# Kernel tuning notes

Measured on AMD Instinct MI355X. Metric: run time of the kernel, lower is better.

## Reference

```python
import jax, jax.numpy as jnp
import numpy as np

B, LQ, LK = 16, 256, 256
DQ = DK = DV = H = 256


def setup_inputs() -> dict:
    key = jax.random.key(0)
    ks = jax.random.split(key, 7)
    queries = jax.random.normal(ks[0], (B, LQ, DQ), dtype=jnp.float32)
    keys = jax.random.normal(ks[1], (B, LK, DK), dtype=jnp.float32)
    values = jax.random.normal(ks[2], (B, LK, DV), dtype=jnp.float32)
    valid_lens = jax.random.randint(ks[3], (B,), 1, LK + 1).astype(jnp.int32)
    W_q = jax.random.normal(ks[4], (DQ, H), dtype=jnp.float32) / np.sqrt(DQ)
    W_k = jax.random.normal(ks[5], (DK, H), dtype=jnp.float32) / np.sqrt(DK)
    w_v = jax.random.normal(ks[6], (H,), dtype=jnp.float32) / np.sqrt(H)
    return {"queries": queries, "keys": keys, "values": values,
            "valid_lens": valid_lens, "W_q": W_q, "W_k": W_k, "w_v": w_v}


def reference(queries, keys, values, valid_lens, W_q, W_k, w_v):
    # Project queries and keys to the hidden size (no bias)
    q = jnp.einsum('bqd,dh->bqh', queries, W_q)          # (B, Lq, H)
    k = jnp.einsum('bkd,dh->bkh', keys, W_k)             # (B, Lk, H)
    # Broadcast-add, tanh, then contract with w_v -> scores (B, Lq, Lk)
    features = jnp.tanh(q[:, :, None, :] + k[:, None, :, :])  # (B, Lq, Lk, H)
    scores = jnp.einsum('bqkh,h->bqk', features, w_v)
    # Masked softmax over last axis: positions >= valid_len get -1e6
    mask = jnp.arange(scores.shape[-1]) < valid_lens[:, None, None]  # (B,1,Lk) bcast
    scores = jnp.where(mask, scores, jnp.float32(-1e6))
    attn = jax.nn.softmax(scores, axis=-1)
    # Dropout is identity at inference (training=False)
    return jnp.einsum('bqk,bkv->bqv', attn, values)      # (B, Lq, Dv)
```

## Files before the change

kernel.cpp:

```cpp
#include <hip/hip_runtime.h>

using bf16x8 = __attribute__((ext_vector_type(8))) __bf16;
using f32x4  = __attribute__((ext_vector_type(4))) float;
using f32x2  = __attribute__((ext_vector_type(2))) float;
using us8    = __attribute__((ext_vector_type(8))) unsigned short;

#define TWO_LOG2E 2.8853900817779268f
#define LOG2E 1.4426950408889634f

__device__ __forceinline__ unsigned short f2bf(float x) {
  unsigned int u = __float_as_uint(x);
  u = (u + 0x7fffu + ((u >> 16) & 1u)) >> 16;
  return (unsigned short)u;
}
__device__ __forceinline__ float bf2f(unsigned short h) {
  return __uint_as_float(((unsigned int)h) << 16);
}
__device__ __forceinline__ f32x2 pk_fma(f32x2 a, f32x2 b, f32x2 c) {
  return __builtin_elementwise_fma(a, b, c);
}

__global__ __launch_bounds__(256) void tcast_kernel(
    const float* __restrict__ Wq, const float* __restrict__ Wk,
    const float* __restrict__ vals, const float* __restrict__ wv,
    const int* __restrict__ vlens,
    unsigned short* __restrict__ wt_hi, unsigned short* __restrict__ wt_lo,
    unsigned short* __restrict__ vt_hi, unsigned short* __restrict__ vt_lo,
    float* __restrict__ wv2, float* __restrict__ Wsum,
    int* __restrict__ ctr, int* __restrict__ cum) {
  if (blockIdx.x == 0) {
    int t = threadIdx.x;
    wv2[t] = -2.0f * wv[t];
    if (t < 64) {
      float s = wv[t] + wv[t + 64] + wv[t + 128] + wv[t + 192];
#pragma unroll
      for (int off = 1; off < 64; off <<= 1) s += __shfl_xor(s, off, 64);
      if (t == 0) Wsum[0] = s;
    }
    if (t == 0) {
      ctr[0] = 0;
      int c = 0;
      for (int b = 0; b < 16; ++b) {
        cum[b] = c;
        c += ((vlens[b] + 31) >> 5) << 3;
      }
      cum[16] = c;
    }
  }
  __shared__ float tile[32][33];
  int m = blockIdx.x >> 6;
  int ts = blockIdx.x & 63;
  int R0 = (ts >> 3) << 5, C0 = (ts & 7) << 5;
  const float* src = (m == 0) ? Wq : (m == 1) ? Wk : (vals + ((m - 2) << 16));
  int r = threadIdx.x >> 3, c4 = (threadIdx.x & 7) << 2;
  float4 v = *(const float4*)(src + (R0 + r) * 256 + C0 + c4);
  tile[r][c4] = v.x; tile[r][c4 + 1] = v.y; tile[r][c4 + 2] = v.z; tile[r][c4 + 3] = v.w;
  __syncthreads();
  float o0 = tile[c4 + 0][r], o1 = tile[c4 + 1][r];
  float o2 = tile[c4 + 2][r], o3 = tile[c4 + 3][r];
  unsigned short h0 = f2bf(o0), h1 = f2bf(o1), h2 = f2bf(o2), h3 = f2bf(o3);
  int base = ((m < 2) ? (m << 16) : ((m - 2) << 16)) + (C0 + r) * 256 + R0 + c4;
  unsigned short* dh = (m < 2) ? wt_hi : vt_hi;
  unsigned short* dl = (m < 2) ? wt_lo : vt_lo;
  *(ushort4*)(dh + base) = make_ushort4(h0, h1, h2, h3);
  *(ushort4*)(dl + base) = make_ushort4(f2bf(o0 - bf2f(h0)), f2bf(o1 - bf2f(h1)),
                                        f2bf(o2 - bf2f(h2)), f2bf(o3 - bf2f(h3)));
}

__global__ __launch_bounds__(256, 4) void proj_kernel(
    const float* __restrict__ q, const float* __restrict__ kk,
    const unsigned short* __restrict__ w_hi, const unsigned short* __restrict__ w_lo,
    const int* __restrict__ vlens, float* __restrict__ Rq, float* __restrict__ RkT) {
  int wave = threadIdx.x >> 6, lane = threadIdx.x & 63;
  int mt = (blockIdx.x << 1) + (wave & 1);
  int m0 = mt << 4;
  int g = mt >> 8;
  if (g) {
    int bb = (m0 >> 8) & 15;
    if ((m0 & 255) >= vlens[bb]) return;
  }
  int r = lane & 15, qd = lane >> 4;
  int row = m0 + r;
  const float* A = (g == 0) ? (q + row * 256) : (kk + (row - 4096) * 256);
  int nbase = (blockIdx.y << 6) + ((wave >> 1) << 5);
  int boff0 = (g << 16) + (nbase + r) * 256 + qd * 8;
  int boff1 = boff0 + (16 << 8);
  f32x4 acc0 = {0.f, 0.f, 0.f, 0.f}, acc1 = {0.f, 0.f, 0.f, 0.f};
#pragma unroll
  for (int kh = 0; kh < 2; ++kh) {
    bf16x8 ah[4], al[4];
#pragma unroll
    for (int s = 0; s < 4; ++s) {
      const float* p = A + qd * 8 + (kh * 4 + s) * 32;
      float4 f0 = *(const float4*)p;
      float4 f1 = *(const float4*)(p + 4);
      float fv[8] = {f0.x, f0.y, f0.z, f0.w, f1.x, f1.y, f1.z, f1.w};
#pragma unroll
      for (int j = 0; j < 8; ++j) {
        __bf16 h = (__bf16)fv[j];
        ah[s][j] = h;
        al[s][j] = (__bf16)(fv[j] - (float)h);
      }
    }
#pragma unroll
    for (int s = 0; s < 4; ++s) {
      int off = (kh * 4 + s) * 32;
      bf16x8 bh0 = *(const bf16x8*)(w_hi + boff0 + off);
      bf16x8 bl0 = *(const bf16x8*)(w_lo + boff0 + off);
      acc0 = __builtin_amdgcn_mfma_f32_16x16x32_bf16(ah[s], bh0, acc0, 0, 0, 0);
      acc0 = __builtin_amdgcn_mfma_f32_16x16x32_bf16(ah[s], bl0, acc0, 0, 0, 0);
      acc0 = __builtin_amdgcn_mfma_f32_16x16x32_bf16(al[s], bh0, acc0, 0, 0, 0);
      bf16x8 bh1 = *(const bf16x8*)(w_hi + boff1 + off);
      bf16x8 bl1 = *(const bf16x8*)(w_lo + boff1 + off);
      acc1 = __builtin_amdgcn_mfma_f32_16x16x32_bf16(ah[s], bh1, acc1, 0, 0, 0);
      acc1 = __builtin_amdgcn_mfma_f32_16x16x32_bf16(ah[s], bl1, acc1, 0, 0, 0);
      acc1 = __builtin_amdgcn_mfma_f32_16x16x32_bf16(al[s], bh1, acc1, 0, 0, 0);
    }
  }
#pragma unroll
  for (int tI = 0; tI < 2; ++tI) {
    f32x4 acc = tI ? acc1 : acc0;
    int n0 = nbase + (tI << 4);
    f32x4 ex;
#pragma unroll
    for (int i = 0; i < 4; ++i) {
      float l = acc[i] * TWO_LOG2E;
      l = fminf(fmaxf(l, -27.f), 27.f);
      ex[i] = __builtin_amdgcn_exp2f(l);
    }
    if (g == 0) {
#pragma unroll
      for (int i = 0; i < 4; ++i)
        Rq[(m0 + qd * 4 + i) * 256 + n0 + r] = ex[i];
    } else {
      int b = (m0 >> 8) & 15;
      int kloc = (m0 & 255) + qd * 4;
      *(f32x4*)(RkT + (b << 16) + (n0 + r) * 256 + kloc) = ex;
    }
  }
}

__global__ __launch_bounds__(256, 2) void scores_kernel(
    const float* __restrict__ Rq, const float* __restrict__ RkT,
    const float* __restrict__ wv2, const float* __restrict__ Wsum,
    const int* __restrict__ cum, int* __restrict__ ctr,
    float* __restrict__ sc) {
  __shared__ __align__(16) float rqs[32 * 76];
  __shared__ __align__(16) float kT[64 * 34];
  __shared__ int s_item;
  const int t = threadIdx.x;
  const int tq = t >> 4, tk = t & 15;
  const int sr = t >> 3, shb = (t & 7) << 3;
  const int hrow = t >> 2, kq = (t & 3) << 3;
  const int total = cum[16];
  const float ws = Wsum[0];

  for (;;) {
    __syncthreads();
    if (t == 0) s_item = atomicAdd(ctr, 1);
    __syncthreads();
    const int w = s_item;
    if (w >= total) return;
    int b = 0;
    while (cum[b + 1] <= w) ++b;
    const int local = w - cum[b];
    const int k0 = (local >> 3) << 5;
    const int q0 = (local & 7) << 5;
    const int qrow = (b << 8) + q0;
    f32x2 a0 = {0.f, 0.f}, a1 = {0.f, 0.f};

    for (int hc = 0; hc < 4; ++hc) {
      if (hc) __syncthreads();
      const float* gq = Rq + (qrow + sr) * 256 + (hc << 6) + shb;
      *(float4*)(rqs + sr * 76 + shb)     = *(const float4*)gq;
      *(float4*)(rqs + sr * 76 + shb + 4) = *(const float4*)(gq + 4);
      const float* gk = RkT + (b << 16) + ((hc << 6) + hrow) * 256 + k0 + kq;
      *(float4*)(kT + hrow * 34 + kq)     = *(const float4*)gk;
      *(float4*)(kT + hrow * 34 + kq + 4) = *(const float4*)(gk + 4);
      __syncthreads();
#pragma unroll 2
      for (int h = 0; h < 64; h += 4) {
        f32x4 qa = *(const f32x4*)(rqs + tq * 76 + h);
        f32x4 qb = *(const f32x4*)(rqs + (tq + 16) * 76 + h);
        f32x4 wm = *(const f32x4*)(wv2 + (hc << 6) + h);
#pragma unroll
        for (int j = 0; j < 4; ++j) {
          f32x2 rk = *(const f32x2*)(kT + (h + j) * 34 + (tk << 1));
          f32x2 wj = (f32x2)(wm[j]);
          f32x2 d0 = pk_fma(rk, (f32x2)(qa[j]), (f32x2)(1.0f));
          f32x2 d1 = pk_fma(rk, (f32x2)(qb[j]), (f32x2)(1.0f));
          f32x2 r0, r1;
          r0.x = __uint_as_float(0x7EF311C3u - __float_as_uint(d0.x));
          r0.y = __uint_as_float(0x7EF311C3u - __float_as_uint(d0.y));
          r1.x = __uint_as_float(0x7EF311C3u - __float_as_uint(d1.x));
          r1.y = __uint_as_float(0x7EF311C3u - __float_as_uint(d1.y));
          r0 = r0 * pk_fma(-d0, r0, (f32x2)(2.0f));
          r1 = r1 * pk_fma(-d1, r1, (f32x2)(2.0f));
          a0 = pk_fma(r0, wj, a0);
          a1 = pk_fma(r1, wj, a1);
        }
      }
    }
    a0 += (f32x2)(ws);
    a1 += (f32x2)(ws);
    *(f32x2*)(sc + ((qrow + tq) << 8) + k0 + (tk << 1)) = a0;
    *(f32x2*)(sc + ((qrow + tq + 16) << 8) + k0 + (tk << 1)) = a1;
  }
}

__global__ __launch_bounds__(256) void av_fused_kernel(
    const float* __restrict__ sc, const int* __restrict__ vlens,
    const unsigned short* __restrict__ vhi, const unsigned short* __restrict__ vlo,
    float* __restrict__ out) {
  __shared__ __align__(16) unsigned short athi[16 * 264];
  const int wave = threadIdx.x >> 6, lane = threadIdx.x & 63;
  const int b = blockIdx.x;
  const int m0 = blockIdx.y << 4;
  const int vl = vlens[b];

  {
    int row = (wave << 2) + (lane & 3);
    int c0 = (lane >> 2) << 4;
    const float* srow = sc + ((b << 8) + m0 + row) * 256 + c0;
    float4 x0 = *(const float4*)(srow);
    float4 x1 = *(const float4*)(srow + 4);
    float4 x2 = *(const float4*)(srow + 8);
    float4 x3 = *(const float4*)(srow + 12);
    float p[16] = {x0.x, x0.y, x0.z, x0.w, x1.x, x1.y, x1.z, x1.w,
                   x2.x, x2.y, x2.z, x2.w, x3.x, x3.y, x3.z, x3.w};
#pragma unroll
    for (int i = 0; i < 16; ++i)
      if (c0 + i >= vl) p[i] = -1e6f;
    float mx = p[0];
#pragma unroll
    for (int i = 1; i < 16; ++i) mx = fmaxf(mx, p[i]);
#pragma unroll
    for (int off = 4; off <= 32; off <<= 1) mx = fmaxf(mx, __shfl_xor(mx, off, 64));
    float sm = 0.f;
#pragma unroll
    for (int i = 0; i < 16; ++i) {
      p[i] = __builtin_amdgcn_exp2f((p[i] - mx) * LOG2E);
      sm += p[i];
    }
#pragma unroll
    for (int off = 4; off <= 32; off <<= 1) sm += __shfl_xor(sm, off, 64);
    float rs = __builtin_amdgcn_rcpf(sm);
    us8 vh[2];
#pragma unroll
    for (int i = 0; i < 16; ++i) vh[i >> 3][i & 7] = f2bf(p[i] * rs);
    *(us8*)(athi + row * 264 + c0)     = vh[0];
    *(us8*)(athi + row * 264 + c0 + 8) = vh[1];
  }
  __syncthreads();

  const int r = lane & 15, qd = lane >> 4;
  const int smax = (vl + 31) >> 5;
  const int nb = wave << 6;
  const int boff = (b << 16) + (nb + r) * 256 + qd * 8;
  f32x4 acc[4] = {{0.f,0.f,0.f,0.f},{0.f,0.f,0.f,0.f},
                  {0.f,0.f,0.f,0.f},{0.f,0.f,0.f,0.f}};
  for (int s = 0; s < smax; ++s) {
    bf16x8 pa = *(const bf16x8*)(athi + r * 264 + qd * 8 + s * 32);
#pragma unroll
    for (int tI = 0; tI < 4; ++tI) {
      bf16x8 bh = *(const bf16x8*)(vhi + boff + (tI << 12) + s * 32);
      bf16x8 bl = *(const bf16x8*)(vlo + boff + (tI << 12) + s * 32);
      acc[tI] = __builtin_amdgcn_mfma_f32_16x16x32_bf16(pa, bh, acc[tI], 0, 0, 0);
      acc[tI] = __builtin_amdgcn_mfma_f32_16x16x32_bf16(pa, bl, acc[tI], 0, 0, 0);
    }
  }
#pragma unroll
  for (int tI = 0; tI < 4; ++tI)
#pragma unroll
    for (int i = 0; i < 4; ++i)
      out[(b << 16) + (m0 + qd * 4 + i) * 256 + nb + (tI << 4) + r] = acc[tI][i];
}

extern "C" void kernel_launch(void* const* d_in, const int* in_sizes, int n_in,
                              void* d_out, int out_size, void* d_ws, size_t ws_size,
                              hipStream_t stream) {
  const float* queries = (const float*)d_in[0];
  const float* keys    = (const float*)d_in[1];
  const float* values  = (const float*)d_in[2];
  const int*   vlens   = (const int*)d_in[3];
  const float* Wq      = (const float*)d_in[4];
  const float* Wk      = (const float*)d_in[5];
  const float* wv      = (const float*)d_in[6];
  float* out = (float*)d_out;
  char* ws = (char*)d_ws;

  unsigned short* wt_hi = (unsigned short*)(ws + 0);
  unsigned short* wt_lo = (unsigned short*)(ws + 262144);
  unsigned short* vt_hi = (unsigned short*)(ws + 524288);
  unsigned short* vt_lo = (unsigned short*)(ws + 2621440);
  float*          Rq    = (float*)(ws + 4718592);
  float*          RkT   = (float*)(ws + 8912896);
  float*          sc    = (float*)(ws + 13107200);
  float*          wv2   = (float*)(ws + 17301504);
  float*          Wsum  = (float*)(ws + 17302528);
  int*            ctr   = (int*)(ws + 17302532);
  int*            cum   = (int*)(ws + 17302536);

  tcast_kernel<<<1152, 256, 0, stream>>>(Wq, Wk, values, wv, vlens,
                                         wt_hi, wt_lo, vt_hi, vt_lo, wv2, Wsum,
                                         ctr, cum);
  proj_kernel<<<dim3(256, 4), 256, 0, stream>>>(queries, keys, wt_hi, wt_lo,
                                                vlens, Rq, RkT);
  scores_kernel<<<512, 256, 0, stream>>>(Rq, RkT, wv2, Wsum, cum, ctr, sc);
  av_fused_kernel<<<dim3(16, 16), 256, 0, stream>>>(sc, vlens, vt_hi, vt_lo, out);
}
```

Baseline: 134.3 us.

## Fuse all stages into persistent megakernel with grid-wide barriers

Replaces four kernel launches with one persistent kernel sized to occupancy, separating stages with atomic grid barriers. The values transpose/cast is moved into the dynamic work queue of the scores stage so it overlaps score computation, and the AV stage is split into quarter-width column tiles to raise parallelism. This removes launch gaps and idle tails between kernels, at the cost of spin barriers, a memset launch, and reliance on all blocks being co-resident.

```diff
diff --git a/kernel.cpp b/kernel.cpp
--- a/kernel.cpp
+++ b/kernel.cpp
@@ -20,16 +20,35 @@
   return __builtin_elementwise_fma(a, b, c);
 }
 
-__global__ __launch_bounds__(256) void tcast_kernel(
-    const float* __restrict__ Wq, const float* __restrict__ Wk,
+__device__ __forceinline__ void gsync(int* bar, int idx, int nblk) {
+  __syncthreads();
+  if (threadIdx.x == 0) {
+    __threadfence();
+    __hip_atomic_fetch_add(bar + idx, 1, __ATOMIC_ACQ_REL, __HIP_MEMORY_SCOPE_AGENT);
+    while (__hip_atomic_load(bar + idx, __ATOMIC_ACQUIRE, __HIP_MEMORY_SCOPE_AGENT) < nblk)
+      __builtin_amdgcn_s_sleep(2);
+  }
+  __syncthreads();
+}
+
+__global__ __launch_bounds__(256, 4) void mega_kernel(
+    const float* __restrict__ q, const float* __restrict__ kk,
     const float* __restrict__ vals, const float* __restrict__ wv,
     const int* __restrict__ vlens,
+    const float* __restrict__ Wq, const float* __restrict__ Wk,
     unsigned short* __restrict__ wt_hi, unsigned short* __restrict__ wt_lo,
     unsigned short* __restrict__ vt_hi, unsigned short* __restrict__ vt_lo,
-    float* __restrict__ wv2, float* __restrict__ Wsum,
-    int* __restrict__ ctr, int* __restrict__ cum) {
+    float* __restrict__ wv2, float* __restrict__ Wsum, int* __restrict__ cum,
+    float* __restrict__ Rq, float* __restrict__ RkT, float* __restrict__ sc,
+    float* __restrict__ out, int* __restrict__ bar) {
+  __shared__ __align__(16) char smem[18448];
+  float* rqs   = (float*)smem;
+  float* kT    = (float*)(smem + 9728);
+  int*   s_item = (int*)(smem + 18432);
+  const int nblk = gridDim.x;
+  const int t = threadIdx.x;
+
   if (blockIdx.x == 0) {
-    int t = threadIdx.x;
     wv2[t] = -2.0f * wv[t];
     if (t < 64) {
       float s = wv[t] + wv[t + 64] + wv[t + 128] + wv[t + 192];
@@ -38,7 +57,6 @@
       if (t == 0) Wsum[0] = s;
     }
     if (t == 0) {
-      ctr[0] = 0;
       int c = 0;
       for (int b = 0; b < 16; ++b) {
         cum[b] = c;
@@ -47,233 +65,238 @@
       cum[16] = c;
     }
   }
-  __shared__ float tile[32][33];
-  int m = blockIdx.x >> 6;
-  int ts = blockIdx.x & 63;
-  int R0 = (ts >> 3) << 5, C0 = (ts & 7) << 5;
-  const float* src = (m == 0) ? Wq : (m == 1) ? Wk : (vals + ((m - 2) << 16));
-  int r = threadIdx.x >> 3, c4 = (threadIdx.x & 7) << 2;
-  float4 v = *(const float4*)(src + (R0 + r) * 256 + C0 + c4);
-  tile[r][c4] = v.x; tile[r][c4 + 1] = v.y; tile[r][c4 + 2] = v.z; tile[r][c4 + 3] = v.w;
-  __syncthreads();
-  float o0 = tile[c4 + 0][r], o1 = tile[c4 + 1][r];
-  float o2 = tile[c4 + 2][r], o3 = tile[c4 + 3][r];
-  unsigned short h0 = f2bf(o0), h1 = f2bf(o1), h2 = f2bf(o2), h3 = f2bf(o3);
-  int base = ((m < 2) ? (m << 16) : ((m - 2) << 16)) + (C0 + r) * 256 + R0 + c4;
-  unsigned short* dh = (m < 2) ? wt_hi : vt_hi;
-  unsigned short* dl = (m < 2) ? wt_lo : vt_lo;
-  *(ushort4*)(dh + base) = make_ushort4(h0, h1, h2, h3);
-  *(ushort4*)(dl + base) = make_ushort4(f2bf(o0 - bf2f(h0)), f2bf(o1 - bf2f(h1)),
-                                        f2bf(o2 - bf2f(h2)), f2bf(o3 - bf2f(h3)));
-}
-
-__global__ __launch_bounds__(256, 4) void proj_kernel(
-    const float* __restrict__ q, const float* __restrict__ kk,
-    const unsigned short* __restrict__ w_hi, const unsigned short* __restrict__ w_lo,
-    const int* __restrict__ vlens, float* __restrict__ Rq, float* __restrict__ RkT) {
-  int wave = threadIdx.x >> 6, lane = threadIdx.x & 63;
-  int mt = (blockIdx.x << 1) + (wave & 1);
-  int m0 = mt << 4;
-  int g = mt >> 8;
-  if (g) {
-    int bb = (m0 >> 8) & 15;
-    if ((m0 & 255) >= vlens[bb]) return;
-  }
-  int r = lane & 15, qd = lane >> 4;
-  int row = m0 + r;
-  const float* A = (g == 0) ? (q + row * 256) : (kk + (row - 4096) * 256);
-  int nbase = (blockIdx.y << 6) + ((wave >> 1) << 5);
-  int boff0 = (g << 16) + (nbase + r) * 256 + qd * 8;
-  int boff1 = boff0 + (16 << 8);
-  f32x4 acc0 = {0.f, 0.f, 0.f, 0.f}, acc1 = {0.f, 0.f, 0.f, 0.f};
-#pragma unroll
-  for (int kh = 0; kh < 2; ++kh) {
-    bf16x8 ah[4], al[4];
-#pragma unroll
-    for (int s = 0; s < 4; ++s) {
-      const float* p = A + qd * 8 + (kh * 4 + s) * 32;
-      float4 f0 = *(const float4*)p;
-      float4 f1 = *(const float4*)(p + 4);
-      float fv[8] = {f0.x, f0.y, f0.z, f0.w, f1.x, f1.y, f1.z, f1.w};
-#pragma unroll
-      for (int j = 0; j < 8; ++j) {
-        __bf16 h = (__bf16)fv[j];
-        ah[s][j] = h;
-        al[s][j] = (__bf16)(fv[j] - (float)h);
-      }
-    }
-#pragma unroll
-    for (int s = 0; s < 4; ++s) {
-      int off = (kh * 4 + s) * 32;
-      bf16x8 bh0 = *(const bf16x8*)(w_hi + boff0 + off);
-      bf16x8 bl0 = *(const bf16x8*)(w_lo + boff0 + off);
-      acc0 = __builtin_amdgcn_mfma_f32_16x16x32_bf16(ah[s], bh0, acc0, 0, 0, 0);
-      acc0 = __builtin_amdgcn_mfma_f32_16x16x32_bf16(ah[s], bl0, acc0, 0, 0, 0);
-      acc0 = __builtin_amdgcn_mfma_f32_16x16x32_bf16(al[s], bh0, acc0, 0, 0, 0);
-      bf16x8 bh1 = *(const bf16x8*)(w_hi + boff1 + off);
-      bf16x8 bl1 = *(const bf16x8*)(w_lo + boff1 + off);
-      acc1 = __builtin_amdgcn_mfma_f32_16x16x32_bf16(ah[s], bh1, acc1, 0, 0, 0);
-      acc1 = __builtin_amdgcn_mfma_f32_16x16x32_bf16(ah[s], bl1, acc1, 0, 0, 0);
-      acc1 = __builtin_amdgcn_mfma_f32_16x16x32_bf16(al[s], bh1, acc1, 0, 0, 0);
-    }
-  }
-#pragma unroll
-  for (int tI = 0; tI < 2; ++tI) {
-    f32x4 acc = tI ? acc1 : acc0;
-    int n0 = nbase + (tI << 4);
-    f32x4 ex;
-#pragma unroll
-    for (int i = 0; i < 4; ++i) {
-      float l = acc[i] * TWO_LOG2E;
-      l = fminf(fmaxf(l, -27.f), 27.f);
-      ex[i] = __builtin_amdgcn_exp2f(l);
-    }
-    if (g == 0) {
-#pragma unroll
-      for (int i = 0; i < 4; ++i)
-        Rq[(m0 + qd * 4 + i) * 256 + n0 + r] = ex[i];
-    } else {
-      int b = (m0 >> 8) & 15;
-      int kloc = (m0 & 255) + qd * 4;
-      *(f32x4*)(RkT + (b << 16) + (n0 + r) * 256 + kloc) = ex;
-    }
-  }
-}
-
-__global__ __launch_bounds__(256, 2) void scores_kernel(
-    const float* __restrict__ Rq, const float* __restrict__ RkT,
-    const float* __restrict__ wv2, const float* __restrict__ Wsum,
-    const int* __restrict__ cum, int* __restrict__ ctr,
-    float* __restrict__ sc) {
-  __shared__ __align__(16) float rqs[32 * 76];
-  __shared__ __align__(16) float kT[64 * 34];
-  __shared__ int s_item;
-  const int t = threadIdx.x;
-  const int tq = t >> 4, tk = t & 15;
-  const int sr = t >> 3, shb = (t & 7) << 3;
-  const int hrow = t >> 2, kq = (t & 3) << 3;
-  const int total = cum[16];
-  const float ws = Wsum[0];
-
-  for (;;) {
+  if (blockIdx.x < 128) {
+    float (*tile)[33] = (float(*)[33])smem;
+    int m = blockIdx.x >> 6, ts = blockIdx.x & 63;
+    int R0 = (ts >> 3) << 5, C0 = (ts & 7) << 5;
+    const float* src = m ? Wk : Wq;
+    int r = t >> 3, c4 = (t & 7) << 2;
+    float4 v = *(const float4*)(src + (R0 + r) * 256 + C0 + c4);
+    tile[r][c4] = v.x; tile[r][c4 + 1] = v.y; tile[r][c4 + 2] = v.z; tile[r][c4 + 3] = v.w;
     __syncthreads();
-    if (t == 0) s_item = atomicAdd(ctr, 1);
+    float o0 = tile[c4 + 0][r], o1 = tile[c4 + 1][r];
+    float o2 = tile[c4 + 2][r], o3 = tile[c4 + 3][r];
+    unsigned short h0 = f2bf(o0), h1 = f2bf(o1), h2 = f2bf(o2), h3 = f2bf(o3);
+    int base = (m << 16) + (C0 + r) * 256 + R0 + c4;
+    *(ushort4*)(wt_hi + base) = make_ushort4(h0, h1, h2, h3);
+    *(ushort4*)(wt_lo + base) = make_ushort4(f2bf(o0 - bf2f(h0)), f2bf(o1 - bf2f(h1)),
+                                             f2bf(o2 - bf2f(h2)), f2bf(o3 - bf2f(h3)));
+  }
+  gsync(bar, 0, nblk);
+
+  for (int j = blockIdx.x; j < 1024; j += nblk) {
+    int wave = t >> 6, lane = t & 63;
+    int mt = ((j & 255) << 1) + (wave & 1);
+    int m0 = mt << 4;
+    int g = mt >> 8;
+    if (g) {
+      int bb = (m0 >> 8) & 15;
+      if ((m0 & 255) >= vlens[bb]) continue;
+    }
+    int r = lane & 15, qd = lane >> 4;
+    int row = m0 + r;
+    const float* A = (g == 0) ? (q + row * 256) : (kk + (row - 4096) * 256);
+    int nbase = ((j >> 8) << 6) + ((wave >> 1) << 5);
+    int boff0 = (g << 16) + (nbase + r) * 256 + qd * 8;
+    int boff1 = boff0 + (16 << 8);
+    f32x4 acc0 = {0.f, 0.f, 0.f, 0.f}, acc1 = {0.f, 0.f, 0.f, 0.f};
+#pragma unroll
+    for (int kh = 0; kh < 2; ++kh) {
+      bf16x8 ah[4], al[4];
+#pragma unroll
+      for (int s = 0; s < 4; ++s) {
+        const float* p = A + qd * 8 + (kh * 4 + s) * 32;
+        float4 f0 = *(const float4*)p;
+        float4 f1 = *(const float4*)(p + 4);
+        float fv[8] = {f0.x, f0.y, f0.z, f0.w, f1.x, f1.y, f1.z, f1.w};
+#pragma unroll
+        for (int jj = 0; jj < 8; ++jj) {
+          __bf16 h = (__bf16)fv[jj];
+          ah[s][jj] = h;
+          al[s][jj] = (__bf16)(fv[jj] - (float)h);
+        }
+      }
+#pragma unroll
+      for (int s = 0; s < 4; ++s) {
+        int off = (kh * 4 + s) * 32;
+        bf16x8 bh0 = *(const bf16x8*)(wt_hi + boff0 + off);
+        bf16x8 bl0 = *(const bf16x8*)(wt_lo + boff0 + off);
+        acc0 = __builtin_amdgcn_mfma_f32_16x16x32_bf16(ah[s], bh0, acc0, 0, 0, 0);
+        acc0 = __builtin_amdgcn_mfma_f32_16x16x32_bf16(ah[s], bl0, acc0, 0, 0, 0);
+        acc0 = __builtin_amdgcn_mfma_f32_16x16x32_bf16(al[s], bh0, acc0, 0, 0, 0);
+        bf16x8 bh1 = *(const bf16x8*)(wt_hi + boff1 + off);
+        bf16x8 bl1 = *(const bf16x8*)(wt_lo + boff1 + off);
+        acc1 = __builtin_amdgcn_mfma_f32_16x16x32_bf16(ah[s], bh1, acc1, 0, 0, 0);
+        acc1 = __builtin_amdgcn_mfma_f32_16x16x32_bf16(ah[s], bl1, acc1, 0, 0, 0);
+        acc1 = __builtin_amdgcn_mfma_f32_16x16x32_bf16(al[s], bh1, acc1, 0, 0, 0);
+      }
+    }
+#pragma unroll
+    for (int tI = 0; tI < 2; ++tI) {
+      f32x4 acc = tI ? acc1 : acc0;
+      int n0 = nbase + (tI << 4);
+      f32x4 ex;
+#pragma unroll
+      for (int i = 0; i < 4; ++i) {
+        float l = acc[i] * TWO_LOG2E;
+        l = fminf(fmaxf(l, -27.f), 27.f);
+        ex[i] = __builtin_amdgcn_exp2f(l);
+      }
+      if (g == 0) {
+#pragma unroll
+        for (int i = 0; i < 4; ++i)
+          Rq[(m0 + qd * 4 + i) * 256 + n0 + r] = ex[i];
+      } else {
+        int b = (m0 >> 8) & 15;
+        int kloc = (m0 & 255) + qd * 4;
+        *(f32x4*)(RkT + (b << 16) + (n0 + r) * 256 + kloc) = ex;
+      }
+    }
+  }
+  gsync(bar, 1, nblk);
+
+  {
+    const int tq = t >> 4, tk = t & 15;
+    const int sr = t >> 3, shb = (t & 7) << 3;
+    const int hrow = t >> 2, kq = (t & 3) << 3;
+    int* ctr = bar + 3;
+    const int S = cum[16];
+    const int total = S + 1024;
+    const float wsum = Wsum[0];
+
+    for (;;) {
+      __syncthreads();
+      if (t == 0) s_item[0] = atomicAdd(ctr, 1);
+      __syncthreads();
+      const int w = s_item[0];
+      if (w >= total) break;
+      if (w < S) {
+        int b = 0;
+        while (cum[b + 1] <= w) ++b;
+        const int local = w - cum[b];
+        const int k0 = (local >> 3) << 5;
+        const int q0 = (local & 7) << 5;
+        const int qrow = (b << 8) + q0;
+        f32x2 a0 = {0.f, 0.f}, a1 = {0.f, 0.f};
+
+        for (int hc = 0; hc < 4; ++hc) {
+          if (hc) __syncthreads();
+          const float* gq = Rq + (qrow + sr) * 256 + (hc << 6) + shb;
+          *(float4*)(rqs + sr * 76 + shb)     = *(const float4*)gq;
+          *(float4*)(rqs + sr * 76 + shb + 4) = *(const float4*)(gq + 4);
+          const float* gk = RkT + (b << 16) + ((hc << 6) + hrow) * 256 + k0 + kq;
+          *(float4*)(kT + hrow * 34 + kq)     = *(const float4*)gk;
+          *(float4*)(kT + hrow * 34 + kq + 4) = *(const float4*)(gk + 4);
+          __syncthreads();
+#pragma unroll 2
+          for (int h = 0; h < 64; h += 4) {
+            f32x4 qa = *(const f32x4*)(rqs + tq * 76 + h);
+            f32x4 qb = *(const f32x4*)(rqs + (tq + 16) * 76 + h);
+            f32x4 wm = *(const f32x4*)(wv2 + (hc << 6) + h);
+#pragma unroll
+            for (int jj = 0; jj < 4; ++jj) {
+              f32x2 rk = *(const f32x2*)(kT + (h + jj) * 34 + (tk << 1));
+              f32x2 wj = (f32x2)(wm[jj]);
+              f32x2 d0 = pk_fma(rk, (f32x2)(qa[jj]), (f32x2)(1.0f));
+              f32x2 d1 = pk_fma(rk, (f32x2)(qb[jj]), (f32x2)(1.0f));
+              f32x2 r0, r1;
+              r0.x = __uint_as_float(0x7EF311C3u - __float_as_uint(d0.x));
+              r0.y = __uint_as_float(0x7EF311C3u - __float_as_uint(d0.y));
+              r1.x = __uint_as_float(0x7EF311C3u - __float_as_uint(d1.x));
+              r1.y = __uint_as_float(0x7EF311C3u - __float_as_uint(d1.y));
+              r0 = r0 * pk_fma(-d0, r0, (f32x2)(2.0f));
+              r1 = r1 * pk_fma(-d1, r1, (f32x2)(2.0f));
+              a0 = pk_fma(r0, wj, a0);
+              a1 = pk_fma(r1, wj, a1);
+            }
+          }
+        }
+        a0 += (f32x2)(wsum);
+        a1 += (f32x2)(wsum);
+        *(f32x2*)(sc + ((qrow + tq) << 8) + k0 + (tk << 1)) = a0;
+        *(f32x2*)(sc + ((qrow + tq + 16) << 8) + k0 + (tk << 1)) = a1;
+      } else {
+        float (*tile)[33] = (float(*)[33])smem;
+        int jv = w - S;
+        int m = jv >> 6, ts = jv & 63;
+        int R0 = (ts >> 3) << 5, C0 = (ts & 7) << 5;
+        const float* src = vals + (m << 16);
+        int r = t >> 3, c4 = (t & 7) << 2;
+        float4 v = *(const float4*)(src + (R0 + r) * 256 + C0 + c4);
+        tile[r][c4] = v.x; tile[r][c4 + 1] = v.y; tile[r][c4 + 2] = v.z; tile[r][c4 + 3] = v.w;
+        __syncthreads();
+        float o0 = tile[c4 + 0][r], o1 = tile[c4 + 1][r];
+        float o2 = tile[c4 + 2][r], o3 = tile[c4 + 3][r];
+        unsigned short h0 = f2bf(o0), h1 = f2bf(o1), h2 = f2bf(o2), h3 = f2bf(o3);
+        int base = (m << 16) + (C0 + r) * 256 + R0 + c4;
+        *(ushort4*)(vt_hi + base) = make_ushort4(h0, h1, h2, h3);
+        *(ushort4*)(vt_lo + base) = make_ushort4(f2bf(o0 - bf2f(h0)), f2bf(o1 - bf2f(h1)),
+                                                 f2bf(o2 - bf2f(h2)), f2bf(o3 - bf2f(h3)));
+      }
+    }
+  }
+  gsync(bar, 2, nblk);
+
+  for (int j = blockIdx.x; j < 1024; j += nblk) {
     __syncthreads();
-    const int w = s_item;
-    if (w >= total) return;
-    int b = 0;
-    while (cum[b + 1] <= w) ++b;
-    const int local = w - cum[b];
-    const int k0 = (local >> 3) << 5;
-    const int q0 = (local & 7) << 5;
-    const int qrow = (b << 8) + q0;
-    f32x2 a0 = {0.f, 0.f}, a1 = {0.f, 0.f};
-
-    for (int hc = 0; hc < 4; ++hc) {
-      if (hc) __syncthreads();
-      const float* gq = Rq + (qrow + sr) * 256 + (hc << 6) + shb;
-      *(float4*)(rqs + sr * 76 + shb)     = *(const float4*)gq;
-      *(float4*)(rqs + sr * 76 + shb + 4) = *(const float4*)(gq + 4);
-      const float* gk = RkT + (b << 16) + ((hc << 6) + hrow) * 256 + k0 + kq;
-      *(float4*)(kT + hrow * 34 + kq)     = *(const float4*)gk;
-      *(float4*)(kT + hrow * 34 + kq + 4) = *(const float4*)(gk + 4);
-      __syncthreads();
-#pragma unroll 2
-      for (int h = 0; h < 64; h += 4) {
-        f32x4 qa = *(const f32x4*)(rqs + tq * 76 + h);
-        f32x4 qb = *(const f32x4*)(rqs + (tq + 16) * 76 + h);
-        f32x4 wm = *(const f32x4*)(wv2 + (hc << 6) + h);
-#pragma unroll
-        for (int j = 0; j < 4; ++j) {
-          f32x2 rk = *(const f32x2*)(kT + (h + j) * 34 + (tk << 1));
-          f32x2 wj = (f32x2)(wm[j]);
-          f32x2 d0 = pk_fma(rk, (f32x2)(qa[j]), (f32x2)(1.0f));
-          f32x2 d1 = pk_fma(rk, (f32x2)(qb[j]), (f32x2)(1.0f));
-          f32x2 r0, r1;
-          r0.x = __uint_as_float(0x7EF311C3u - __float_as_uint(d0.x));
-          r0.y = __uint_as_float(0x7EF311C3u - __float_as_uint(d0.y));
-          r1.x = __uint_as_float(0x7EF311C3u - __float_as_uint(d1.x));
-          r1.y = __uint_as_float(0x7EF311C3u - __float_as_uint(d1.y));
-          r0 = r0 * pk_fma(-d0, r0, (f32x2)(2.0f));
-          r1 = r1 * pk_fma(-d1, r1, (f32x2)(2.0f));
-          a0 = pk_fma(r0, wj, a0);
-          a1 = pk_fma(r1, wj, a1);
-        }
-      }
-    }
-    a0 += (f32x2)(ws);
-    a1 += (f32x2)(ws);
-    *(f32x2*)(sc + ((qrow + tq) << 8) + k0 + (tk << 1)) = a0;
-    *(f32x2*)(sc + ((qrow + tq + 16) << 8) + k0 + (tk << 1)) = a1;
-  }
-}
-
-__global__ __launch_bounds__(256) void av_fused_kernel(
-    const float* __restrict__ sc, const int* __restrict__ vlens,
-    const unsigned short* __restrict__ vhi, const unsigned short* __restrict__ vlo,
-    float* __restrict__ out) {
-  __shared__ __align__(16) unsigned short athi[16 * 264];
-  const int wave = threadIdx.x >> 6, lane = threadIdx.x & 63;
-  const int b = blockIdx.x;
-  const int m0 = blockIdx.y << 4;
-  const int vl = vlens[b];
-
-  {
-    int row = (wave << 2) + (lane & 3);
-    int c0 = (lane >> 2) << 4;
-    const float* srow = sc + ((b << 8) + m0 + row) * 256 + c0;
-    float4 x0 = *(const float4*)(srow);
-    float4 x1 = *(const float4*)(srow + 4);
-    float4 x2 = *(const float4*)(srow + 8);
-    float4 x3 = *(const float4*)(srow + 12);
-    float p[16] = {x0.x, x0.y, x0.z, x0.w, x1.x, x1.y, x1.z, x1.w,
-                   x2.x, x2.y, x2.z, x2.w, x3.x, x3.y, x3.z, x3.w};
-#pragma unroll
-    for (int i = 0; i < 16; ++i)
-      if (c0 + i >= vl) p[i] = -1e6f;
-    float mx = p[0];
-#pragma unroll
-    for (int i = 1; i < 16; ++i) mx = fmaxf(mx, p[i]);
-#pragma unroll
-    for (int off = 4; off <= 32; off <<= 1) mx = fmaxf(mx, __shfl_xor(mx, off, 64));
-    float sm = 0.f;
-#pragma unroll
-    for (int i = 0; i < 16; ++i) {
-      p[i] = __builtin_amdgcn_exp2f((p[i] - mx) * LOG2E);
-      sm += p[i];
-    }
-#pragma unroll
-    for (int off = 4; off <= 32; off <<= 1) sm += __shfl_xor(sm, off, 64);
-    float rs = __builtin_amdgcn_rcpf(sm);
-    us8 vh[2];
-#pragma unroll
-    for (int i = 0; i < 16; ++i) vh[i >> 3][i & 7] = f2bf(p[i] * rs);
-    *(us8*)(athi + row * 264 + c0)     = vh[0];
-    *(us8*)(athi + row * 264 + c0 + 8) = vh[1];
-  }
-  __syncthreads();
-
-  const int r = lane & 15, qd = lane >> 4;
-  const int smax = (vl + 31) >> 5;
-  const int nb = wave << 6;
-  const int boff = (b << 16) + (nb + r) * 256 + qd * 8;
-  f32x4 acc[4] = {{0.f,0.f,0.f,0.f},{0.f,0.f,0.f,0.f},
-                  {0.f,0.f,0.f,0.f},{0.f,0.f,0.f,0.f}};
-  for (int s = 0; s < smax; ++s) {
-    bf16x8 pa = *(const bf16x8*)(athi + r * 264 + qd * 8 + s * 32);
-#pragma unroll
-    for (int tI = 0; tI < 4; ++tI) {
-      bf16x8 bh = *(const bf16x8*)(vhi + boff + (tI << 12) + s * 32);
-      bf16x8 bl = *(const bf16x8*)(vlo + boff + (tI << 12) + s * 32);
-      acc[tI] = __builtin_amdgcn_mfma_f32_16x16x32_bf16(pa, bh, acc[tI], 0, 0, 0);
-      acc[tI] = __builtin_amdgcn_mfma_f32_16x16x32_bf16(pa, bl, acc[tI], 0, 0, 0);
-    }
-  }
-#pragma unroll
-  for (int tI = 0; tI < 4; ++tI)
+    unsigned short* athi = (unsigned short*)smem;
+    const int wave = t >> 6, lane = t & 63;
+    const int b = j & 15;
+    const int m0 = ((j >> 4) & 15) << 4;
+    const int quad = j >> 8;
+    const int vl = vlens[b];
+
+    {
+      int row = (wave << 2) + (lane & 3);
+      int c0 = (lane >> 2) << 4;
+      const float* srow = sc + ((b << 8) + m0 + row) * 256 + c0;
+      float4 x0 = *(const float4*)(srow);
+      float4 x1 = *(const float4*)(srow + 4);
+      float4 x2 = *(const float4*)(srow + 8);
+      float4 x3 = *(const float4*)(srow + 12);
+      float p[16] = {x0.x, x0.y, x0.z, x0.w, x1.x, x1.y, x1.z, x1.w,
+                     x2.x, x2.y, x2.z, x2.w, x3.x, x3.y, x3.z, x3.w};
+#pragma unroll
+      for (int i = 0; i < 16; ++i)
+        if (c0 + i >= vl) p[i] = -1e6f;
+      float mx = p[0];
+#pragma unroll
+      for (int i = 1; i < 16; ++i) mx = fmaxf(mx, p[i]);
+#pragma unroll
+      for (int off = 4; off <= 32; off <<= 1) mx = fmaxf(mx, __shfl_xor(mx, off, 64));
+      float sm = 0.f;
+#pragma unroll
+      for (int i = 0; i < 16; ++i) {
+        p[i] = __builtin_amdgcn_exp2f((p[i] - mx) * LOG2E);
+        sm += p[i];
+      }
+#pragma unroll
+      for (int off = 4; off <= 32; off <<= 1) sm += __shfl_xor(sm, off, 64);
+      float rs = __builtin_amdgcn_rcpf(sm);
+      us8 vh[2];
+#pragma unroll
+      for (int i = 0; i < 16; ++i) vh[i >> 3][i & 7] = f2bf(p[i] * rs);
+      *(us8*)(athi + row * 264 + c0)     = vh[0];
+      *(us8*)(athi + row * 264 + c0 + 8) = vh[1];
+    }
+    __syncthreads();
+
+    const int r = lane & 15, qd = lane >> 4;
+    const int smax = (vl + 31) >> 5;
+    const int n0 = (quad << 6) + (wave << 4);
+    const int boff = (b << 16) + (n0 + r) * 256 + qd * 8;
+    f32x4 acc = {0.f, 0.f, 0.f, 0.f};
+    for (int s = 0; s < smax; ++s) {
+      bf16x8 pa = *(const bf16x8*)(athi + r * 264 + qd * 8 + s * 32);
+      bf16x8 bh = *(const bf16x8*)(vt_hi + boff + s * 32);
+      bf16x8 bl = *(const bf16x8*)(vt_lo + boff + s * 32);
+      acc = __builtin_amdgcn_mfma_f32_16x16x32_bf16(pa, bh, acc, 0, 0, 0);
+      acc = __builtin_amdgcn_mfma_f32_16x16x32_bf16(pa, bl, acc, 0, 0, 0);
+    }
 #pragma unroll
     for (int i = 0; i < 4; ++i)
-      out[(b << 16) + (m0 + qd * 4 + i) * 256 + nb + (tI << 4) + r] = acc[tI][i];
+      out[(b << 16) + (m0 + qd * 4 + i) * 256 + n0 + r] = acc[i];
+  }
 }
 
 extern "C" void kernel_launch(void* const* d_in, const int* in_sizes, int n_in,
@@ -298,14 +321,29 @@
   float*          sc    = (float*)(ws + 13107200);
   float*          wv2   = (float*)(ws + 17301504);
   float*          Wsum  = (float*)(ws + 17302528);
-  int*            ctr   = (int*)(ws + 17302532);
   int*            cum   = (int*)(ws + 17302536);
-
-  tcast_kernel<<<1152, 256, 0, stream>>>(Wq, Wk, values, wv, vlens,
-                                         wt_hi, wt_lo, vt_hi, vt_lo, wv2, Wsum,
-                                         ctr, cum);
-  proj_kernel<<<dim3(256, 4), 256, 0, stream>>>(queries, keys, wt_hi, wt_lo,
-                                                vlens, Rq, RkT);
-  scores_kernel<<<512, 256, 0, stream>>>(Rq, RkT, wv2, Wsum, cum, ctr, sc);
-  av_fused_kernel<<<dim3(16, 16), 256, 0, stream>>>(sc, vlens, vt_hi, vt_lo, out);
-}
+  int*            bar   = (int*)(ws + 17302604);
+
+  static int nblk = 0;
+  if (nblk == 0) {
+    int per = 0;
+    if (hipOccupancyMaxActiveBlocksPerMultiprocessor(&per, mega_kernel, 256, 0) != hipSuccess
+        || per < 1) per = 1;
+    if (per > 4) per = 4;
+    int cus = 256;
+    hipDeviceProp_t prop;
+    int dev = 0;
+    if (hipGetDevice(&dev) == hipSuccess &&
+        hipGetDeviceProperties(&prop, dev) == hipSuccess &&
+        prop.multiProcessorCount > 0)
+      cus = prop.multiProcessorCount;
+    long g = (long)per * cus;
+    nblk = (int)(g > 1024 ? 1024 : g);
+    if (nblk < 1) nblk = 1;
+  }
+
+  hipMemsetAsync(ws + 17302604, 0, 16, stream);
+  mega_kernel<<<nblk, 256, 0, stream>>>(queries, keys, values, wv, vlens, Wq, Wk,
+                                        wt_hi, wt_lo, vt_hi, vt_lo, wv2, Wsum, cum,
+                                        Rq, RkT, sc, out, bar);
+}
```

Result: slower. 425.6 us (+216.9%).

## Fuse scores, masked softmax and AV into one per-query-tile kernel

Applied to the files above, without the earlier changes.

Merges the scores kernel and the softmax/AV kernel into one kernel with one block per (batch, 16-query tile). Each block loops over only the valid key tiles, keeps scores in shared memory, then runs softmax and the bf16 MFMA AV product. This removes the global score buffer round trip, one launch, and the atomic work-queue setup. In exchange, each thread now computes one query row instead of two, so there is less instruction-level parallelism. The grid is fixed at 256 blocks with no dynamic balancing, so batches with long valid lengths become the critical path.

```diff
diff --git a/kernel.cpp b/kernel.cpp
--- a/kernel.cpp
+++ b/kernel.cpp
@@ -23,11 +23,9 @@
 __global__ __launch_bounds__(256) void tcast_kernel(
     const float* __restrict__ Wq, const float* __restrict__ Wk,
     const float* __restrict__ vals, const float* __restrict__ wv,
-    const int* __restrict__ vlens,
     unsigned short* __restrict__ wt_hi, unsigned short* __restrict__ wt_lo,
     unsigned short* __restrict__ vt_hi, unsigned short* __restrict__ vt_lo,
-    float* __restrict__ wv2, float* __restrict__ Wsum,
-    int* __restrict__ ctr, int* __restrict__ cum) {
+    float* __restrict__ wv2, float* __restrict__ Wsum) {
   if (blockIdx.x == 0) {
     int t = threadIdx.x;
     wv2[t] = -2.0f * wv[t];
@@ -36,15 +34,6 @@
 #pragma unroll
       for (int off = 1; off < 64; off <<= 1) s += __shfl_xor(s, off, 64);
       if (t == 0) Wsum[0] = s;
-    }
-    if (t == 0) {
-      ctr[0] = 0;
-      int c = 0;
-      for (int b = 0; b < 16; ++b) {
-        cum[b] = c;
-        c += ((vlens[b] + 31) >> 5) << 3;
-      }
-      cum[16] = c;
     }
   }
   __shared__ float tile[32][33];
@@ -140,88 +129,69 @@
   }
 }
 
-__global__ __launch_bounds__(256, 2) void scores_kernel(
+__global__ __launch_bounds__(256) void sav_kernel(
     const float* __restrict__ Rq, const float* __restrict__ RkT,
     const float* __restrict__ wv2, const float* __restrict__ Wsum,
-    const int* __restrict__ cum, int* __restrict__ ctr,
-    float* __restrict__ sc) {
-  __shared__ __align__(16) float rqs[32 * 76];
+    const int* __restrict__ vlens,
+    const unsigned short* __restrict__ vhi, const unsigned short* __restrict__ vlo,
+    float* __restrict__ out) {
+  __shared__ __align__(16) float rqs[16 * 260];
   __shared__ __align__(16) float kT[64 * 34];
-  __shared__ int s_item;
+  __shared__ __align__(16) float scs[16 * 264];
+  unsigned short* athi = (unsigned short*)rqs;
   const int t = threadIdx.x;
+  const int b = blockIdx.x;
+  const int q0 = blockIdx.y << 4;
+  const int qrow = (b << 8) + q0;
+  const int vl = vlens[b];
+  const int nkt = (vl + 31) >> 5;
+  const float wsum = Wsum[0];
+
+  {
+    int row = t >> 4, c0 = (t & 15) << 4;
+    const float* g = Rq + (qrow + row) * 256 + c0;
+#pragma unroll
+    for (int i = 0; i < 4; ++i)
+      *(float4*)(rqs + row * 260 + c0 + i * 4) = *(const float4*)(g + i * 4);
+  }
   const int tq = t >> 4, tk = t & 15;
-  const int sr = t >> 3, shb = (t & 7) << 3;
   const int hrow = t >> 2, kq = (t & 3) << 3;
-  const int total = cum[16];
-  const float ws = Wsum[0];
-
-  for (;;) {
-    __syncthreads();
-    if (t == 0) s_item = atomicAdd(ctr, 1);
-    __syncthreads();
-    const int w = s_item;
-    if (w >= total) return;
-    int b = 0;
-    while (cum[b + 1] <= w) ++b;
-    const int local = w - cum[b];
-    const int k0 = (local >> 3) << 5;
-    const int q0 = (local & 7) << 5;
-    const int qrow = (b << 8) + q0;
-    f32x2 a0 = {0.f, 0.f}, a1 = {0.f, 0.f};
-
+
+  for (int kt = 0; kt < nkt; ++kt) {
+    const int k0 = kt << 5;
+    f32x2 a0 = {0.f, 0.f};
     for (int hc = 0; hc < 4; ++hc) {
-      if (hc) __syncthreads();
-      const float* gq = Rq + (qrow + sr) * 256 + (hc << 6) + shb;
-      *(float4*)(rqs + sr * 76 + shb)     = *(const float4*)gq;
-      *(float4*)(rqs + sr * 76 + shb + 4) = *(const float4*)(gq + 4);
+      __syncthreads();
       const float* gk = RkT + (b << 16) + ((hc << 6) + hrow) * 256 + k0 + kq;
       *(float4*)(kT + hrow * 34 + kq)     = *(const float4*)gk;
       *(float4*)(kT + hrow * 34 + kq + 4) = *(const float4*)(gk + 4);
       __syncthreads();
 #pragma unroll 2
       for (int h = 0; h < 64; h += 4) {
-        f32x4 qa = *(const f32x4*)(rqs + tq * 76 + h);
-        f32x4 qb = *(const f32x4*)(rqs + (tq + 16) * 76 + h);
+        f32x4 qa = *(const f32x4*)(rqs + tq * 260 + (hc << 6) + h);
         f32x4 wm = *(const f32x4*)(wv2 + (hc << 6) + h);
 #pragma unroll
         for (int j = 0; j < 4; ++j) {
           f32x2 rk = *(const f32x2*)(kT + (h + j) * 34 + (tk << 1));
-          f32x2 wj = (f32x2)(wm[j]);
           f32x2 d0 = pk_fma(rk, (f32x2)(qa[j]), (f32x2)(1.0f));
-          f32x2 d1 = pk_fma(rk, (f32x2)(qb[j]), (f32x2)(1.0f));
-          f32x2 r0, r1;
+          f32x2 r0;
           r0.x = __uint_as_float(0x7EF311C3u - __float_as_uint(d0.x));
           r0.y = __uint_as_float(0x7EF311C3u - __float_as_uint(d0.y));
-          r1.x = __uint_as_float(0x7EF311C3u - __float_as_uint(d1.x));
-          r1.y = __uint_as_float(0x7EF311C3u - __float_as_uint(d1.y));
           r0 = r0 * pk_fma(-d0, r0, (f32x2)(2.0f));
-          r1 = r1 * pk_fma(-d1, r1, (f32x2)(2.0f));
-          a0 = pk_fma(r0, wj, a0);
-          a1 = pk_fma(r1, wj, a1);
+          a0 = pk_fma(r0, (f32x2)(wm[j]), a0);
         }
       }
     }
-    a0 += (f32x2)(ws);
-    a1 += (f32x2)(ws);
-    *(f32x2*)(sc + ((qrow + tq) << 8) + k0 + (tk << 1)) = a0;
-    *(f32x2*)(sc + ((qrow + tq + 16) << 8) + k0 + (tk << 1)) = a1;
-  }
-}
-
-__global__ __launch_bounds__(256) void av_fused_kernel(
-    const float* __restrict__ sc, const int* __restrict__ vlens,
-    const unsigned short* __restrict__ vhi, const unsigned short* __restrict__ vlo,
-    float* __restrict__ out) {
-  __shared__ __align__(16) unsigned short athi[16 * 264];
-  const int wave = threadIdx.x >> 6, lane = threadIdx.x & 63;
-  const int b = blockIdx.x;
-  const int m0 = blockIdx.y << 4;
-  const int vl = vlens[b];
+    a0 += (f32x2)(wsum);
+    *(f32x2*)(scs + tq * 264 + k0 + (tk << 1)) = a0;
+  }
+  __syncthreads();
 
   {
+    const int wave = t >> 6, lane = t & 63;
     int row = (wave << 2) + (lane & 3);
     int c0 = (lane >> 2) << 4;
-    const float* srow = sc + ((b << 8) + m0 + row) * 256 + c0;
+    const float* srow = scs + row * 264 + c0;
     float4 x0 = *(const float4*)(srow);
     float4 x1 = *(const float4*)(srow + 4);
     float4 x2 = *(const float4*)(srow + 8);
@@ -253,27 +223,29 @@
   }
   __syncthreads();
 
-  const int r = lane & 15, qd = lane >> 4;
-  const int smax = (vl + 31) >> 5;
-  const int nb = wave << 6;
-  const int boff = (b << 16) + (nb + r) * 256 + qd * 8;
-  f32x4 acc[4] = {{0.f,0.f,0.f,0.f},{0.f,0.f,0.f,0.f},
-                  {0.f,0.f,0.f,0.f},{0.f,0.f,0.f,0.f}};
-  for (int s = 0; s < smax; ++s) {
-    bf16x8 pa = *(const bf16x8*)(athi + r * 264 + qd * 8 + s * 32);
-#pragma unroll
-    for (int tI = 0; tI < 4; ++tI) {
-      bf16x8 bh = *(const bf16x8*)(vhi + boff + (tI << 12) + s * 32);
-      bf16x8 bl = *(const bf16x8*)(vlo + boff + (tI << 12) + s * 32);
-      acc[tI] = __builtin_amdgcn_mfma_f32_16x16x32_bf16(pa, bh, acc[tI], 0, 0, 0);
-      acc[tI] = __builtin_amdgcn_mfma_f32_16x16x32_bf16(pa, bl, acc[tI], 0, 0, 0);
-    }
-  }
-#pragma unroll
-  for (int tI = 0; tI < 4; ++tI)
-#pragma unroll
-    for (int i = 0; i < 4; ++i)
-      out[(b << 16) + (m0 + qd * 4 + i) * 256 + nb + (tI << 4) + r] = acc[tI][i];
+  {
+    const int wave = t >> 6, lane = t & 63;
+    const int r = lane & 15, qd = lane >> 4;
+    const int nb = wave << 6;
+    const int boff = (b << 16) + (nb + r) * 256 + qd * 8;
+    f32x4 acc[4] = {{0.f,0.f,0.f,0.f},{0.f,0.f,0.f,0.f},
+                    {0.f,0.f,0.f,0.f},{0.f,0.f,0.f,0.f}};
+    for (int s = 0; s < nkt; ++s) {
+      bf16x8 pa = *(const bf16x8*)(athi + r * 264 + qd * 8 + s * 32);
+#pragma unroll
+      for (int tI = 0; tI < 4; ++tI) {
+        bf16x8 bh = *(const bf16x8*)(vhi + boff + (tI << 12) + s * 32);
+        bf16x8 bl = *(const bf16x8*)(vlo + boff + (tI << 12) + s * 32);
+        acc[tI] = __builtin_amdgcn_mfma_f32_16x16x32_bf16(pa, bh, acc[tI], 0, 0, 0);
+        acc[tI] = __builtin_amdgcn_mfma_f32_16x16x32_bf16(pa, bl, acc[tI], 0, 0, 0);
+      }
+    }
+#pragma unroll
+    for (int tI = 0; tI < 4; ++tI)
+#pragma unroll
+      for (int i = 0; i < 4; ++i)
+        out[(b << 16) + (q0 + qd * 4 + i) * 256 + nb + (tI << 4) + r] = acc[tI][i];
+  }
 }
 
 extern "C" void kernel_launch(void* const* d_in, const int* in_sizes, int n_in,
@@ -295,17 +267,13 @@
   unsigned short* vt_lo = (unsigned short*)(ws + 2621440);
   float*          Rq    = (float*)(ws + 4718592);
   float*          RkT   = (float*)(ws + 8912896);
-  float*          sc    = (float*)(ws + 13107200);
-  float*          wv2   = (float*)(ws + 17301504);
-  float*          Wsum  = (float*)(ws + 17302528);
-  int*            ctr   = (int*)(ws + 17302532);
-  int*            cum   = (int*)(ws + 17302536);
-
-  tcast_kernel<<<1152, 256, 0, stream>>>(Wq, Wk, values, wv, vlens,
-                                         wt_hi, wt_lo, vt_hi, vt_lo, wv2, Wsum,
-                                         ctr, cum);
+  float*          wv2   = (float*)(ws + 13107200);
+  float*          Wsum  = (float*)(ws + 13108224);
+
+  tcast_kernel<<<1152, 256, 0, stream>>>(Wq, Wk, values, wv,
+                                         wt_hi, wt_lo, vt_hi, vt_lo, wv2, Wsum);
   proj_kernel<<<dim3(256, 4), 256, 0, stream>>>(queries, keys, wt_hi, wt_lo,
                                                 vlens, Rq, RkT);
-  scores_kernel<<<512, 256, 0, stream>>>(Rq, RkT, wv2, Wsum, cum, ctr, sc);
-  av_fused_kernel<<<dim3(16, 16), 256, 0, stream>>>(sc, vlens, vt_hi, vt_lo, out);
-}
+  sav_kernel<<<dim3(16, 16), 256, 0, stream>>>(Rq, RkT, wv2, Wsum, vlens,
+                                               vt_hi, vt_lo, out);
+}
```

New measurement: 175.7 us. 1.31x slower.
